# Kernel tuning notes

Measured on AMD Instinct MI355X. Metric: run time of the kernel, lower is better.

The kernel has to match this reference:

```python
import jax, jax.numpy as jnp
import numpy as np

N_QUBITS = 6
BLOCKS = 3
LATENT = 3
DIM = 1 << N_QUBITS  # 64, state-vector size
BATCH = 131072
INP_DIM = 6  # must equal N_QUBITS (repo applies linear_pre to the n_qubits-dim recon)

# Wire 0 is the most-significant qubit (PennyLane convention).
_idx = np.arange(DIM)
BITS = ((_idx[:, None] >> (N_QUBITS - 1 - np.arange(N_QUBITS))) & 1)  # (64, 6)
# Chain of CZ(k, k+1): all diagonal, fold into one sign vector per block.
CZ_SIGN = jnp.asarray(np.prod(1 - 2 * (BITS[:, :-1] * BITS[:, 1:]), axis=1).astype(np.float32))  # (64,)
Z_SIGNS = jnp.asarray((1 - 2 * BITS).astype(np.float32))  # (64, 6): <Z_k> signs per basis state


def _apply_1q(state, U, wire):
    # state: (B, 64) complex64; U: (2,2) complex64 acting on `wire`
    B = state.shape[0]
    s = state.reshape(B, 1 << wire, 2, 1 << (N_QUBITS - 1 - wire))
    s = jnp.einsum('ij,bxjy->bxiy', U, s)
    return s.reshape(B, DIM)


def _circuit(amps, weights, n_out):
    # AmplitudeEmbedding with normalize=True (x was already unit-normed in torch; idempotent)
    norm = jnp.linalg.norm(amps, axis=1, keepdims=True)
    state = (amps / norm).astype(jnp.complex64)  # (B, 64)
    for j in range(BLOCKS):
        for k in range(N_QUBITS):
            tx = weights[j, k, 0]
            tz = weights[j, k, 1]
            c = jnp.cos(0.5 * tx).astype(jnp.complex64)
            s = jnp.sin(0.5 * tx).astype(jnp.complex64)
            em = jnp.exp(-0.5j * tz).astype(jnp.complex64)
            ep = jnp.exp(0.5j * tz).astype(jnp.complex64)
            # Fused U = RZ(tz) @ RX(tx)
            U = jnp.stack([jnp.stack([em * c, -1j * em * s]),
                           jnp.stack([-1j * ep * s, ep * c])])
            state = _apply_1q(state, U, k)
        state = state * CZ_SIGN  # all CZ gates of the block, fused
    probs = state.real ** 2 + state.imag ** 2  # (B, 64)
    return probs @ Z_SIGNS[:, :n_out]  # expval(PauliZ(k)) for k < n_out


def setup_inputs() -> dict:
    key = jax.random.key(0)
    k1, k2, k3, k4, k5 = jax.random.split(key, 5)
    x = jax.random.normal(k1, (BATCH, INP_DIM), dtype=jnp.float32)
    bound = 1.0 / np.sqrt(INP_DIM)
    W_pre = jax.random.uniform(k2, (DIM, INP_DIM), minval=-bound, maxval=bound, dtype=jnp.float32)
    b_pre = jax.random.uniform(k3, (DIM,), minval=-bound, maxval=bound, dtype=jnp.float32)
    enc_w = jax.random.normal(k4, (BLOCKS, N_QUBITS, 3), dtype=jnp.float32) * 0.01
    dec_w = jax.random.normal(k5, (BLOCKS, N_QUBITS, 3), dtype=jnp.float32) * 0.01
    return {'x': x, 'W_pre': W_pre, 'b_pre': b_pre, 'enc_w': enc_w, 'dec_w': dec_w}


def reference(x, W_pre, b_pre, enc_w, dec_w):
    h = jnp.tanh(x @ W_pre.T + b_pre)                     # (B, 64)
    latent = _circuit(h, enc_w, LATENT)                    # (B, 3)
    padded = jnp.zeros((x.shape[0], DIM), jnp.float32).at[:, :LATENT].set(latent)
    recon = _circuit(padded, dec_w, N_QUBITS)              # (B, 6)
    reconstructed = jnp.tanh(recon @ W_pre.T + b_pre)      # (B, 64)
    return reconstructed, latent
```

## Files before the change

### kernel.cpp

```cpp
#include <hip/hip_runtime.h>

#define BATCH 131072


__device__ __forceinline__ float fast_tanh(float v) {
    float e = __expf(2.0f * v);
    return 1.0f - 2.0f / (e + 1.0f);
}

template <int CTRL>
__device__ __forceinline__ float dppf(float v) {
    return __int_as_float(__builtin_amdgcn_update_dpp(
        0, __float_as_int(v), CTRL, 0xF, 0xF, true));
}
#define DPP_XOR1 0xB1
#define DPP_XOR2 0x4E

__global__ __launch_bounds__(256) void prep_kernel(const float* __restrict__ enc_w,
                                                   const float* __restrict__ dec_w,
                                                   float* __restrict__ ws) {
    __shared__ float gt[18][8];
    __shared__ float Sr[64][8];
    __shared__ float Si[64][8];
    const int t = threadIdx.x;

    if (t < 18) {
        float tx = dec_w[t * 3 + 0];
        float tz = dec_w[t * 3 + 1];
        float c = cosf(0.5f * tx), s = sinf(0.5f * tx);
        float ch = cosf(0.5f * tz), sh = sinf(0.5f * tz);
        gt[t][0] = c * ch;  gt[t][1] = -c * sh;
        gt[t][2] = -s * sh; gt[t][3] = -s * ch;
        gt[t][4] = s * sh;  gt[t][5] = -s * ch;
        gt[t][6] = c * ch;  gt[t][7] = c * sh;
    }

    const int cl = t & 7;
    const int pr = t >> 3;
    float* fSr = &Sr[0][0];
    float* fSi = &Si[0][0];
    for (int f = t; f < 512; f += 256) {
        int r = f >> 3, c = f & 7;
        fSr[f] = (r == c && c < 3) ? 1.0f : 0.0f;
        fSi[f] = 0.0f;
    }

    for (int bb = 0; bb < 3; ++bb) {
        for (int w = 0; w < 6; ++w) {
            __syncthreads();
            int g = bb * 6 + w;
            int p = 5 - w;
            float u00r = gt[g][0], u00i = gt[g][1], u01r = gt[g][2], u01i = gt[g][3];
            float u10r = gt[g][4], u10i = gt[g][5], u11r = gt[g][6], u11i = gt[g][7];
            int r0 = ((pr >> p) << (p + 1)) | (pr & ((1 << p) - 1));
            int r1 = r0 | (1 << p);
            float ar = Sr[r0][cl], ai = Si[r0][cl];
            float br = Sr[r1][cl], bi = Si[r1][cl];
            Sr[r0][cl] = u00r * ar - u00i * ai + u01r * br - u01i * bi;
            Si[r0][cl] = u00r * ai + u00i * ar + u01r * bi + u01i * br;
            Sr[r1][cl] = u10r * ar - u10i * ai + u11r * br - u11i * bi;
            Si[r1][cl] = u10r * ai + u10i * ar + u11r * bi + u11i * br;
        }
        __syncthreads();
        for (int f = t; f < 512; f += 256) {
            int r = f >> 3;
            if (__popc(r & (r >> 1)) & 1) {
                fSr[f] = -fSr[f];
                fSi[f] = -fSi[f];
            }
        }
    }
    __syncthreads();

    if (t < 54) {
        int k = t / 9, d = (t % 9) / 3, e = t % 3;
        float acc = 0.0f;
        for (int r = 0; r < 64; ++r) {
            float term = Sr[r][d] * Sr[r][e] + Si[r][d] * Si[r][e];
            acc += ((r >> (5 - k)) & 1) ? -term : term;
        }
        ws[t] = acc;
    }

    if (t < 18) {
        float tx = enc_w[t * 3 + 0];
        ws[64 + 2 * t] = cosf(0.5f * tx);
        ws[65 + 2 * t] = sinf(0.5f * tx);
    }

    if (t >= 64 && t < 256) {
        int idx = t - 64;
        int bb = idx >> 6, r = idx & 63;
        float phi = 0.0f;
        for (int k = 0; k < 6; ++k) {
            float tz = enc_w[(bb * 6 + k) * 3 + 1];
            phi += ((r >> (5 - k)) & 1) ? 0.5f * tz : -0.5f * tz;
        }
        float sgn = (__popc(r & (r >> 1)) & 1) ? -1.0f : 1.0f;
        ws[128 + bb * 128 + 2 * r] = sgn * cosf(phi);
        ws[129 + bb * 128 + 2 * r] = sgn * sinf(phi);
    }
}

template <int Q>
__device__ __forceinline__ void rx_local(float* sr, float* si, float c, float s) {
#pragma unroll
    for (int k = 0; k < 8; ++k) {
        int lo = k & ((1 << Q) - 1);
        int m0 = ((k >> Q) << (Q + 1)) | lo;
        int m1 = m0 | (1 << Q);
        float ar = sr[m0], ai = si[m0], br = sr[m1], bi = si[m1];
        sr[m0] = c * ar + s * bi;
        si[m0] = c * ai - s * br;
        sr[m1] = c * br + s * ai;
        si[m1] = c * bi - s * ar;
    }
}

template <int CTRL>
__device__ __forceinline__ void rx_exch(float* sr, float* si, float c, float s) {
#pragma unroll
    for (int m = 0; m < 16; ++m) {
        float pr = dppf<CTRL>(sr[m]);
        float pi = dppf<CTRL>(si[m]);
        float mr = sr[m], mi = si[m];
        sr[m] = c * mr + s * pi;
        si[m] = c * mi - s * pr;
    }
}

__global__ __launch_bounds__(256, 4) void qae_main(const float* __restrict__ x,
                                                   const float* __restrict__ Wp,
                                                   const float* __restrict__ bp,
                                                   const float* __restrict__ ws,
                                                   float* __restrict__ out) {
    __shared__ float sW[512];
    __shared__ float sD[384];
    __shared__ float sLat[192];

    const int t = threadIdx.x;
    const int bl = t >> 2;
    const int sub = t & 3;

    for (int f = t; f < 512; f += 256) {
        int i = f >> 3, c = f & 7;
        sW[f] = (c < 6) ? Wp[i * 6 + c] : ((c == 6) ? bp[i] : 0.0f);
    }
    for (int f = t; f < 384; f += 256) sD[f] = ws[128 + f];
    __syncthreads();

    const size_t b = (size_t)blockIdx.x * 64 + bl;
    const float* xp = x + b * 6;
    float2 x01 = *(const float2*)(xp);
    float2 x23 = *(const float2*)(xp + 2);
    float2 x45 = *(const float2*)(xp + 4);
    float xv[6] = {x01.x, x01.y, x23.x, x23.y, x45.x, x45.y};

    float sr[16], si[16];
    float S = 0.0f;
    const float* wbase = &sW[sub * 8];
#pragma unroll
    for (int m = 0; m < 16; ++m) {
        const float* wr = wbase + m * 32;
        float4 w0 = *(const float4*)wr;
        float4 w1 = *(const float4*)(wr + 4);
        float a = w1.z + w0.x * xv[0] + w0.y * xv[1] + w0.z * xv[2] +
                  w0.w * xv[3] + w1.x * xv[4] + w1.y * xv[5];
        float th = fast_tanh(a);
        sr[m] = th;
        si[m] = 0.0f;
        S += th * th;
    }
    S += dppf<DPP_XOR1>(S);
    S += dppf<DPP_XOR2>(S);
    float invS = __builtin_amdgcn_rcpf(S);

#pragma unroll 1
    for (int bb = 0; bb < 3; ++bb) {
        const float* rx = ws + 64 + 12 * bb;
        rx_local<3>(sr, si, rx[0], rx[1]);
        rx_local<2>(sr, si, rx[2], rx[3]);
        rx_local<1>(sr, si, rx[4], rx[5]);
        rx_local<0>(sr, si, rx[6], rx[7]);
        rx_exch<DPP_XOR2>(sr, si, rx[8], rx[9]);
        rx_exch<DPP_XOR1>(sr, si, rx[10], rx[11]);
        const float* dgl = &sD[bb * 128 + sub * 2];
#pragma unroll
        for (int m = 0; m < 16; ++m) {
            float2 d = *(const float2*)&dgl[8 * m];
            float ar = sr[m], ai = si[m];
            sr[m] = d.x * ar - d.y * ai;
            si[m] = d.x * ai + d.y * ar;
        }
    }

    float l0 = 0.0f, l1 = 0.0f, l2 = 0.0f;
#pragma unroll
    for (int m = 0; m < 16; ++m) {
        float p = sr[m] * sr[m] + si[m] * si[m];
        l0 += (m & 8) ? -p : p;
        l1 += (m & 4) ? -p : p;
        l2 += (m & 2) ? -p : p;
    }
    l0 += dppf<DPP_XOR1>(l0); l0 += dppf<DPP_XOR2>(l0);
    l1 += dppf<DPP_XOR1>(l1); l1 += dppf<DPP_XOR2>(l1);
    l2 += dppf<DPP_XOR1>(l2); l2 += dppf<DPP_XOR2>(l2);
    l0 *= invS; l1 *= invS; l2 *= invS;

    float r2 = l0 * l0 + l1 * l1 + l2 * l2;
    float invr2 = __builtin_amdgcn_rcpf(r2);
    float lv[3] = {l0, l1, l2};
    float rec[6];
#pragma unroll
    for (int k = 0; k < 6; ++k) {
        float acc = 0.0f;
#pragma unroll
        for (int d = 0; d < 3; ++d)
#pragma unroll
            for (int e = 0; e < 3; ++e) acc += ws[k * 9 + d * 3 + e] * lv[d] * lv[e];
        rec[k] = acc * invr2;
    }

    if (sub == 0) {
        sLat[bl * 3 + 0] = l0;
        sLat[bl * 3 + 1] = l1;
        sLat[bl * 3 + 2] = l2;
    }
    __syncthreads();
    if (t < 192) out[(size_t)BATCH * 64 + (size_t)blockIdx.x * 192 + t] = sLat[t];

    const size_t ob = b * 64 + sub * 16;
#pragma unroll
    for (int q = 0; q < 4; ++q) {
        float vals[4];
#pragma unroll
        for (int c2 = 0; c2 < 4; ++c2) {
            const float* wr = &sW[(sub * 16 + q * 4 + c2) * 8];
            float4 w0 = *(const float4*)wr;
            float4 w1 = *(const float4*)(wr + 4);
            float a = w1.z + w0.x * rec[0] + w0.y * rec[1] + w0.z * rec[2] +
                      w0.w * rec[3] + w1.x * rec[4] + w1.y * rec[5];
            vals[c2] = fast_tanh(a);
        }
        float4 o = {vals[0], vals[1], vals[2], vals[3]};
        *(float4*)&out[ob + q * 4] = o;
    }
}

extern "C" void kernel_launch(void* const* d_in, const int* in_sizes, int n_in,
                              void* d_out, int out_size, void* d_ws, size_t ws_size,
                              hipStream_t stream) {
    const float* x   = (const float*)d_in[0];
    const float* Wp  = (const float*)d_in[1];
    const float* bpv = (const float*)d_in[2];
    const float* enc = (const float*)d_in[3];
    const float* dec = (const float*)d_in[4];
    float* out = (float*)d_out;
    float* ws  = (float*)d_ws;

    prep_kernel<<<1, 256, 0, stream>>>(enc, dec, ws);
    qae_main<<<(BATCH * 4) / 256, 256, 0, stream>>>(x, Wp, bpv, ws, out);
}
```

Baseline: 118.5 us.

## Pack state amplitudes into float2 vectors for packed FP32 math

```diff
diff --git a/kernel.cpp b/kernel.cpp
--- a/kernel.cpp
+++ b/kernel.cpp
@@ -1,6 +1,8 @@
 #include <hip/hip_runtime.h>
 
 #define BATCH 131072
+
+typedef float v2f __attribute__((ext_vector_type(2)));
 
 
 __device__ __forceinline__ float fast_tanh(float v) {
@@ -15,6 +17,8 @@
 }
 #define DPP_XOR1 0xB1
 #define DPP_XOR2 0x4E
+
+__device__ __forceinline__ v2f swap2(v2f v) { return __builtin_shufflevector(v, v, 1, 0); }
 
 __global__ __launch_bounds__(256) void prep_kernel(const float* __restrict__ enc_w,
                                                    const float* __restrict__ dec_w,
@@ -102,40 +106,42 @@
     }
 }
 
-template <int Q>
-__device__ __forceinline__ void rx_local(float* sr, float* si, float c, float s) {
-#pragma unroll
-    for (int k = 0; k < 8; ++k) {
-        int lo = k & ((1 << Q) - 1);
-        int m0 = ((k >> Q) << (Q + 1)) | lo;
-        int m1 = m0 | (1 << Q);
-        float ar = sr[m0], ai = si[m0], br = sr[m1], bi = si[m1];
-        sr[m0] = c * ar + s * bi;
-        si[m0] = c * ai - s * br;
-        sr[m1] = c * br + s * ai;
-        si[m1] = c * bi - s * ar;
+template <int MASK>
+__device__ __forceinline__ void rx_pairs(v2f* zr, v2f* zi, float c, float s) {
+#pragma unroll
+    for (int j = 0; j < 8; ++j) {
+        if (j & MASK) continue;
+        int j1 = j | MASK;
+        v2f ar = zr[j], ai = zi[j], br = zr[j1], bi = zi[j1];
+        zr[j]  = c * ar + s * bi;
+        zi[j]  = c * ai - s * br;
+        zr[j1] = c * br + s * ai;
+        zi[j1] = c * bi - s * ar;
     }
 }
 
 template <int CTRL>
-__device__ __forceinline__ void rx_exch(float* sr, float* si, float c, float s) {
-#pragma unroll
-    for (int m = 0; m < 16; ++m) {
-        float pr = dppf<CTRL>(sr[m]);
-        float pi = dppf<CTRL>(si[m]);
-        float mr = sr[m], mi = si[m];
-        sr[m] = c * mr + s * pi;
-        si[m] = c * mi - s * pr;
-    }
-}
-
-__global__ __launch_bounds__(256, 4) void qae_main(const float* __restrict__ x,
-                                                   const float* __restrict__ Wp,
-                                                   const float* __restrict__ bp,
-                                                   const float* __restrict__ ws,
-                                                   float* __restrict__ out) {
-    __shared__ float sW[512];
-    __shared__ float sD[384];
+__device__ __forceinline__ void rx_exch2(v2f* zr, v2f* zi, float c, float s) {
+#pragma unroll
+    for (int j = 0; j < 8; ++j) {
+        v2f pr, pi;
+        pr.x = dppf<CTRL>(zr[j].x);
+        pr.y = dppf<CTRL>(zr[j].y);
+        pi.x = dppf<CTRL>(zi[j].x);
+        pi.y = dppf<CTRL>(zi[j].y);
+        v2f mr = zr[j], mi = zi[j];
+        zr[j] = c * mr + s * pi;
+        zi[j] = c * mi - s * pr;
+    }
+}
+
+__global__ __launch_bounds__(256) void qae_main(const float* __restrict__ x,
+                                                const float* __restrict__ Wp,
+                                                const float* __restrict__ bp,
+                                                const float* __restrict__ ws,
+                                                float* __restrict__ out) {
+    __shared__ float sW[540];
+    __shared__ float sD[256];
     __shared__ float sLat[192];
 
     const int t = threadIdx.x;
@@ -143,10 +149,21 @@
     const int sub = t & 3;
 
     for (int f = t; f < 512; f += 256) {
-        int i = f >> 3, c = f & 7;
-        sW[f] = (c < 6) ? Wp[i * 6 + c] : ((c == 6) ? bp[i] : 0.0f);
-    }
-    for (int f = t; f < 384; f += 256) sD[f] = ws[128 + f];
+        int g = f >> 4, e = f & 15;
+        int j = g >> 2, su = g & 3;
+        float val;
+        if (e < 12)      { int row = 8 * j + su + 4 * (e & 1); val = Wp[row * 6 + (e >> 1)]; }
+        else if (e < 14) { int row = 8 * j + su + 4 * (e - 12); val = bp[row]; }
+        else val = 0.0f;
+        sW[g * 16 + j * 4 + e] = val;
+    }
+    if (t < 128) {
+        int bb = t >> 6, r = t & 63;
+        int su = r & 3, m = r >> 2, j = m >> 1, hm = m & 1;
+        int base = ((bb * 8 + j) * 4 + su) * 4;
+        sD[base + hm]     = ws[128 + bb * 128 + 2 * r];
+        sD[base + 2 + hm] = ws[128 + bb * 128 + 2 * r + 1];
+    }
     __syncthreads();
 
     const size_t b = (size_t)blockIdx.x * 64 + bl;
@@ -156,21 +173,28 @@
     float2 x45 = *(const float2*)(xp + 4);
     float xv[6] = {x01.x, x01.y, x23.x, x23.y, x45.x, x45.y};
 
-    float sr[16], si[16];
-    float S = 0.0f;
-    const float* wbase = &sW[sub * 8];
-#pragma unroll
-    for (int m = 0; m < 16; ++m) {
-        const float* wr = wbase + m * 32;
-        float4 w0 = *(const float4*)wr;
-        float4 w1 = *(const float4*)(wr + 4);
-        float a = w1.z + w0.x * xv[0] + w0.y * xv[1] + w0.z * xv[2] +
-                  w0.w * xv[3] + w1.x * xv[4] + w1.y * xv[5];
-        float th = fast_tanh(a);
-        sr[m] = th;
-        si[m] = 0.0f;
-        S += th * th;
-    }
+    v2f zr[8], zi[8];
+    v2f S2 = {0.0f, 0.0f};
+#pragma unroll
+    for (int j = 0; j < 8; ++j) {
+        const float* wb = &sW[(j * 4 + sub) * 16 + j * 4];
+        float4 c0 = *(const float4*)wb;
+        float4 c1 = *(const float4*)(wb + 4);
+        float4 c2 = *(const float4*)(wb + 8);
+        float4 c3 = *(const float4*)(wb + 12);
+        v2f a = {c3.x, c3.y};
+        a += xv[0] * (v2f){c0.x, c0.y};
+        a += xv[1] * (v2f){c0.z, c0.w};
+        a += xv[2] * (v2f){c1.x, c1.y};
+        a += xv[3] * (v2f){c1.z, c1.w};
+        a += xv[4] * (v2f){c2.x, c2.y};
+        a += xv[5] * (v2f){c2.z, c2.w};
+        v2f th = {fast_tanh(a.x), fast_tanh(a.y)};
+        zr[j] = th;
+        zi[j] = (v2f){0.0f, 0.0f};
+        S2 += th * th;
+    }
+    float S = S2.x + S2.y;
     S += dppf<DPP_XOR1>(S);
     S += dppf<DPP_XOR2>(S);
     float invS = __builtin_amdgcn_rcpf(S);
@@ -178,30 +202,41 @@
 #pragma unroll 1
     for (int bb = 0; bb < 3; ++bb) {
         const float* rx = ws + 64 + 12 * bb;
-        rx_local<3>(sr, si, rx[0], rx[1]);
-        rx_local<2>(sr, si, rx[2], rx[3]);
-        rx_local<1>(sr, si, rx[4], rx[5]);
-        rx_local<0>(sr, si, rx[6], rx[7]);
-        rx_exch<DPP_XOR2>(sr, si, rx[8], rx[9]);
-        rx_exch<DPP_XOR1>(sr, si, rx[10], rx[11]);
-        const float* dgl = &sD[bb * 128 + sub * 2];
-#pragma unroll
-        for (int m = 0; m < 16; ++m) {
-            float2 d = *(const float2*)&dgl[8 * m];
-            float ar = sr[m], ai = si[m];
-            sr[m] = d.x * ar - d.y * ai;
-            si[m] = d.x * ai + d.y * ar;
-        }
-    }
-
-    float l0 = 0.0f, l1 = 0.0f, l2 = 0.0f;
-#pragma unroll
-    for (int m = 0; m < 16; ++m) {
-        float p = sr[m] * sr[m] + si[m] * si[m];
-        l0 += (m & 8) ? -p : p;
-        l1 += (m & 4) ? -p : p;
-        l2 += (m & 2) ? -p : p;
-    }
+        rx_pairs<4>(zr, zi, rx[0], rx[1]);
+        rx_pairs<2>(zr, zi, rx[2], rx[3]);
+        rx_pairs<1>(zr, zi, rx[4], rx[5]);
+        {
+            float c = rx[6], s = rx[7];
+#pragma unroll
+            for (int j = 0; j < 8; ++j) {
+                v2f orr = zr[j], oi = zi[j];
+                zr[j] = c * orr + s * swap2(oi);
+                zi[j] = c * oi - s * swap2(orr);
+            }
+        }
+        rx_exch2<DPP_XOR2>(zr, zi, rx[8], rx[9]);
+        rx_exch2<DPP_XOR1>(zr, zi, rx[10], rx[11]);
+        if (bb < 2) {
+#pragma unroll
+            for (int j = 0; j < 8; ++j) {
+                float4 d = *(const float4*)&sD[((bb * 8 + j) * 4 + sub) * 4];
+                v2f dr = {d.x, d.y}, di = {d.z, d.w};
+                v2f orr = zr[j], oi = zi[j];
+                zr[j] = dr * orr - di * oi;
+                zi[j] = dr * oi + di * orr;
+            }
+        }
+    }
+
+    v2f L0 = {0, 0}, L1 = {0, 0}, L2 = {0, 0};
+#pragma unroll
+    for (int j = 0; j < 8; ++j) {
+        v2f p = zr[j] * zr[j] + zi[j] * zi[j];
+        L0 += (j & 4) ? -p : p;
+        L1 += (j & 2) ? -p : p;
+        L2 += (j & 1) ? -p : p;
+    }
+    float l0 = L0.x + L0.y, l1 = L1.x + L1.y, l2 = L2.x + L2.y;
     l0 += dppf<DPP_XOR1>(l0); l0 += dppf<DPP_XOR2>(l0);
     l1 += dppf<DPP_XOR1>(l1); l1 += dppf<DPP_XOR2>(l1);
     l2 += dppf<DPP_XOR1>(l2); l2 += dppf<DPP_XOR2>(l2);
@@ -229,21 +264,33 @@
     __syncthreads();
     if (t < 192) out[(size_t)BATCH * 64 + (size_t)blockIdx.x * 192 + t] = sLat[t];
 
-    const size_t ob = b * 64 + sub * 16;
-#pragma unroll
-    for (int q = 0; q < 4; ++q) {
-        float vals[4];
-#pragma unroll
-        for (int c2 = 0; c2 < 4; ++c2) {
-            const float* wr = &sW[(sub * 16 + q * 4 + c2) * 8];
-            float4 w0 = *(const float4*)wr;
-            float4 w1 = *(const float4*)(wr + 4);
-            float a = w1.z + w0.x * rec[0] + w0.y * rec[1] + w0.z * rec[2] +
-                      w0.w * rec[3] + w1.x * rec[4] + w1.y * rec[5];
-            vals[c2] = fast_tanh(a);
-        }
-        float4 o = {vals[0], vals[1], vals[2], vals[3]};
-        *(float4*)&out[ob + q * 4] = o;
+    const size_t ob = b * 64;
+#pragma unroll
+    for (int jj = 0; jj < 2; ++jj) {
+        int jrow = 2 * sub + jj;
+        float vlo[4], vhi[4];
+#pragma unroll
+        for (int su2 = 0; su2 < 4; ++su2) {
+            int g = jrow * 4 + su2;
+            const float* wb = &sW[g * 16 + jrow * 4];
+            float4 c0 = *(const float4*)wb;
+            float4 c1 = *(const float4*)(wb + 4);
+            float4 c2 = *(const float4*)(wb + 8);
+            float2 b2 = *(const float2*)(wb + 12);
+            v2f a = {b2.x, b2.y};
+            a += rec[0] * (v2f){c0.x, c0.y};
+            a += rec[1] * (v2f){c0.z, c0.w};
+            a += rec[2] * (v2f){c1.x, c1.y};
+            a += rec[3] * (v2f){c1.z, c1.w};
+            a += rec[4] * (v2f){c2.x, c2.y};
+            a += rec[5] * (v2f){c2.z, c2.w};
+            vlo[su2] = fast_tanh(a.x);
+            vhi[su2] = fast_tanh(a.y);
+        }
+        float4 o0 = {vlo[0], vlo[1], vlo[2], vlo[3]};
+        float4 o1 = {vhi[0], vhi[1], vhi[2], vhi[3]};
+        *(float4*)&out[ob + 8 * jrow]     = o0;
+        *(float4*)&out[ob + 8 * jrow + 4] = o1;
     }
 }
 
```

New measurement: 105.4 us. 11.1% less time.
